# Optimization experiments

Measured on AMD Instinct MI355X. Metric: run time of the kernel, lower is better.

Reference implementation:

```python
import jax, jax.numpy as jnp
import numpy as np

WINDOW_SIZE = 128
NEG = -1e9

def setup_inputs() -> dict:
    key = jax.random.key(0)
    kq, kk, kv = jax.random.split(key, 3)
    B, H, T, D = 2, 16, 2048, 64
    q = jax.random.normal(kq, (B, H, T, D), dtype=jnp.float32)
    k = jax.random.normal(kk, (B, H, T, D), dtype=jnp.float32)
    v = jax.random.normal(kv, (B, H, T, D), dtype=jnp.float32)
    return {"q": q, "k": k, "v": v}

def reference(q, k, v):
    # q,k,v: (B, H, T, D)
    D = q.shape[-1]
    Tq, Tk = q.shape[2], k.shape[2]
    scale = 1.0 / jnp.sqrt(jnp.asarray(D, dtype=q.dtype))
    scores = jnp.einsum('bhqd,bhkd->bhqk', q, k) * scale  # (B,H,Tq,Tk)
    dist = jnp.abs(jnp.arange(Tq)[:, None] - jnp.arange(Tk)[None, :])
    window_mask = dist <= WINDOW_SIZE  # (Tq,Tk)
    scores = jnp.where(window_mask[None, None], scores, jnp.asarray(NEG, dtype=scores.dtype))
    attn = jax.nn.softmax(scores, axis=-1)
    output = jnp.einsum('bhqk,bhkd->bhqd', attn, v)
    return (output, attn)
```

## Files before the change

kernel.cpp:

```cpp
#include <hip/hip_runtime.h>
#include <hip/hip_bf16.h>

typedef short bf16x8 __attribute__((ext_vector_type(8)));
typedef short bf16x4 __attribute__((ext_vector_type(4)));
typedef float f32x4 __attribute__((ext_vector_type(4)));

#define T_DIM 2048
#define D_DIM 64
#define WIN 128
#define QBLK 64
#define ACCT 17
#define NEGBIG -1e30f

__device__ __forceinline__ short f2b(float x) {
  __hip_bfloat16 h = __float2bfloat16(x);
  return *reinterpret_cast<short*>(&h);
}
__device__ __forceinline__ float b2f(short s) {
  unsigned u = ((unsigned)(unsigned short)s) << 16;
  return __builtin_bit_cast(float, u);
}
__device__ __forceinline__ bf16x8 cvt8(f32x4 a, f32x4 b) {
  bf16x8 r;
  r[0] = f2b(a[0]); r[1] = f2b(a[1]); r[2] = f2b(a[2]); r[3] = f2b(a[3]);
  r[4] = f2b(b[0]); r[5] = f2b(b[1]); r[6] = f2b(b[2]); r[7] = f2b(b[3]);
  return r;
}
__device__ __forceinline__ int swz(int row, int b) { return row * 640 + (b ^ ((row & 7) << 4)); }

__global__ __launch_bounds__(256, 2) void lsa_one(
    const float* __restrict__ Qg, const float* __restrict__ Kg,
    const float* __restrict__ Vg, float* __restrict__ Og,
    float* __restrict__ Ag) {
  const int tid = threadIdx.x;
  const int work = ((blockIdx.x & 7) << 7) + (blockIdx.x >> 3);
  const int bh = work >> 5;
  const int q0 = (work & 31) * QBLK;
  int kstart = q0 - WIN; if (kstart < 0) kstart = 0;
  int kend = q0 + QBLK + WIN; if (kend > T_DIM) kend = T_DIM;
  const int KW = kend - kstart;
  const int nkt = KW >> 4;

  const float* qptr = Qg + (size_t)bh * (T_DIM * D_DIM);
  const float* kptr = Kg + (size_t)bh * (T_DIM * D_DIM);
  const float* vptr = Vg + (size_t)bh * (T_DIM * D_DIM);
  float* optr = Og + (size_t)bh * (T_DIM * D_DIM);
  float* aptr = Ag + (size_t)bh * ((size_t)T_DIM * T_DIM);

  __shared__ __align__(16) char Vb[D_DIM * 640];
  __shared__ __align__(16) char Pb[QBLK * 640];

  for (int idx = tid; idx < KW * 16; idx += 256) {
    const int r = idx >> 4, c4 = idx & 15;
    f32x4 f = *(const f32x4*)(vptr + (size_t)(kstart + r) * D_DIM + c4 * 4);
    const int d0 = c4 * 4;
    *(short*)(Vb + swz(d0 + 0, r * 2)) = f2b(f[0]);
    *(short*)(Vb + swz(d0 + 1, r * 2)) = f2b(f[1]);
    *(short*)(Vb + swz(d0 + 2, r * 2)) = f2b(f[2]);
    *(short*)(Vb + swz(d0 + 3, r * 2)) = f2b(f[3]);
  }

  const int lane = tid & 63, w = tid >> 6, c = lane & 15, hi = lane >> 4;

  const float* qrow = qptr + (size_t)(q0 + w * 16 + c) * D_DIM + 8 * hi;
  const bf16x8 qb0 = cvt8(*(const f32x4*)qrow, *(const f32x4*)(qrow + 4));
  const bf16x8 qb1 = cvt8(*(const f32x4*)(qrow + 32), *(const f32x4*)(qrow + 36));

  int klo = q0 + w * 16 - WIN - kstart; if (klo < 0) klo = 0;
  const int kt0 = klo >> 4;
  int kt1 = (q0 + w * 16 + 15 + WIN + 1 - kstart + 15) >> 4; if (kt1 > nkt) kt1 = nkt;
  const int s0 = kt0 >> 1, s1 = (kt1 + 1) >> 1;
  const int nlive = kt1 - kt0;

  f32x4 acc[ACCT];
#pragma unroll
  for (int i = 0; i < ACCT; ++i) {
    acc[i] = (f32x4){0.f, 0.f, 0.f, 0.f};
    if (i < nlive) {
      const float* kr = kptr + (size_t)(kstart + (kt0 + i) * 16 + c) * D_DIM + 8 * hi;
      const bf16x8 b0 = cvt8(*(const f32x4*)kr, *(const f32x4*)(kr + 4));
      const bf16x8 b1 = cvt8(*(const f32x4*)(kr + 32), *(const f32x4*)(kr + 36));
      acc[i] = __builtin_amdgcn_mfma_f32_16x16x32_bf16(b0, qb0, acc[i], 0, 0, 0);
      acc[i] = __builtin_amdgcn_mfma_f32_16x16x32_bf16(b1, qb1, acc[i], 0, 0, 0);
    }
  }

  {
    const f32x4 zv = {0.f, 0.f, 0.f, 0.f};
    for (int rr = 0; rr < 16; ++rr) {
      float* dst = aptr + (size_t)(q0 + w * 16 + rr) * T_DIM;
      for (int col = lane * 4; col < kstart; col += 256)
        __builtin_nontemporal_store(zv, (f32x4*)(dst + col));
      for (int col = kend + lane * 4; col < T_DIM; col += 256)
        __builtin_nontemporal_store(zv, (f32x4*)(dst + col));
    }
  }

  const int qr = q0 + w * 16 + c;
  const int kb = kstart + 4 * hi;
  float m = NEGBIG;
#pragma unroll
  for (int i = 0; i < ACCT; ++i)
    if (i < nlive) {
#pragma unroll
      for (int j = 0; j < 4; ++j) {
        float s = acc[i][j] * 0.125f;
        const int kcol = kb + (kt0 + i) * 16 + j;
        int dist = qr - kcol; dist = dist < 0 ? -dist : dist;
        s = (dist <= WIN) ? s : NEGBIG;
        acc[i][j] = s;
        m = fmaxf(m, s);
      }
    }
  m = fmaxf(m, __shfl_xor(m, 16));
  m = fmaxf(m, __shfl_xor(m, 32));
  float sum = 0.f;
#pragma unroll
  for (int i = 0; i < ACCT; ++i)
    if (i < nlive) {
#pragma unroll
      for (int j = 0; j < 4; ++j) {
        const float p = __expf(acc[i][j] - m);
        acc[i][j] = p;
        sum += p;
      }
    }
  sum += __shfl_xor(sum, 16);
  sum += __shfl_xor(sum, 32);
  const float inv = 1.f / sum;

  const int prow = w * 16 + c;
#pragma unroll
  for (int i = 0; i < ACCT; ++i)
    if (i < nlive) {
      bf16x4 pk;
#pragma unroll
      for (int j = 0; j < 4; ++j) pk[j] = f2b(acc[i][j] * inv);
      *(bf16x4*)(Pb + swz(prow, 32 * (kt0 + i) + 8 * hi)) = pk;
    }
  {
    const bf16x4 z4 = {0, 0, 0, 0};
    for (int t = 0; t < kt0; ++t) *(bf16x4*)(Pb + swz(prow, 32 * t + 8 * hi)) = z4;
    for (int t = kt1; t < nkt; ++t) *(bf16x4*)(Pb + swz(prow, 32 * t + 8 * hi)) = z4;
  }

  for (int rr = 0; rr < 16; ++rr) {
    const int r = w * 16 + rr;
    float* dst = aptr + (size_t)(q0 + r) * T_DIM + kstart;
#pragma unroll
    for (int i = 0; i < 5; ++i) {
      const int off = i * 256 + lane * 4;
      if (off < KW) {
        const bf16x4 pv = *(const bf16x4*)(Pb + swz(r, off * 2));
        f32x4 val;
        val[0] = b2f(pv[0]); val[1] = b2f(pv[1]); val[2] = b2f(pv[2]); val[3] = b2f(pv[3]);
        __builtin_nontemporal_store(val, (f32x4*)(dst + off));
      }
    }
  }

  __syncthreads();

  f32x4 ov[4];
#pragma unroll
  for (int dt = 0; dt < 4; ++dt) ov[dt] = (f32x4){0.f, 0.f, 0.f, 0.f};
  for (int s = s0; s < s1; ++s) {
    const bf16x8 pa = *(const bf16x8*)(Pb + swz(w * 16 + c, 64 * s + 16 * hi));
#pragma unroll
    for (int dt = 0; dt < 4; ++dt) {
      const bf16x8 vb = *(const bf16x8*)(Vb + swz(dt * 16 + c, 64 * s + 16 * hi));
      ov[dt] = __builtin_amdgcn_mfma_f32_16x16x32_bf16(pa, vb, ov[dt], 0, 0, 0);
    }
  }
#pragma unroll
  for (int dt = 0; dt < 4; ++dt)
#pragma unroll
    for (int j = 0; j < 4; ++j)
      __builtin_nontemporal_store(
          ov[dt][j], optr + (size_t)(q0 + w * 16 + 4 * hi + j) * D_DIM + dt * 16 + c);
}

extern "C" void kernel_launch(void* const* d_in, const int* in_sizes, int n_in,
                              void* d_out, int out_size, void* d_ws, size_t ws_size,
                              hipStream_t stream) {
  const float* q = (const float*)d_in[0];
  const float* k = (const float*)d_in[1];
  const float* v = (const float*)d_in[2];
  float* out = (float*)d_out;
  float* attn = out + (size_t)2 * 16 * T_DIM * D_DIM;
  lsa_one<<<dim3(2 * 16 * (T_DIM / QBLK)), dim3(256), 0, stream>>>(q, k, v, out, attn);
}
```

Measured before the change: 128.4 us.

## Keep probabilities in registers, store attn directly, feed PV MFMA from accumulators

Removes the shared-memory P buffer. The normalized attention rows are written straight from registers to global memory, and unnormalized bf16 probabilities feed a 16x16x16 MFMA directly from the score accumulator layout. Normalization by 1/sum is deferred to the output store using shuffles. Freeing the P buffer raises launch bounds to 4 blocks per SU, targeting occupancy and fewer LDS round trips. In exchange, the attn stores become 16-byte per-lane scattered writes rather than coalesced row writes, and the change adds manual s_nop hazard padding.

```diff
diff --git a/kernel.cpp b/kernel.cpp
--- a/kernel.cpp
+++ b/kernel.cpp
@@ -16,10 +16,6 @@
   __hip_bfloat16 h = __float2bfloat16(x);
   return *reinterpret_cast<short*>(&h);
 }
-__device__ __forceinline__ float b2f(short s) {
-  unsigned u = ((unsigned)(unsigned short)s) << 16;
-  return __builtin_bit_cast(float, u);
-}
 __device__ __forceinline__ bf16x8 cvt8(f32x4 a, f32x4 b) {
   bf16x8 r;
   r[0] = f2b(a[0]); r[1] = f2b(a[1]); r[2] = f2b(a[2]); r[3] = f2b(a[3]);
@@ -28,7 +24,19 @@
 }
 __device__ __forceinline__ int swz(int row, int b) { return row * 640 + (b ^ ((row & 7) << 4)); }
 
-__global__ __launch_bounds__(256, 2) void lsa_one(
+#if __has_builtin(__builtin_amdgcn_mfma_f32_16x16x16bf16_1k)
+__device__ __forceinline__ f32x4 mfma16(bf16x4 a, bf16x4 b, f32x4 c) {
+  return __builtin_amdgcn_mfma_f32_16x16x16bf16_1k(a, b, c, 0, 0, 0);
+}
+#else
+__device__ __forceinline__ f32x4 mfma16(bf16x4 a, bf16x4 b, f32x4 c) {
+  asm volatile("s_nop 1\n\tv_mfma_f32_16x16x16_bf16 %0, %1, %2, %0"
+               : "+v"(c) : "v"(a), "v"(b));
+  return c;
+}
+#endif
+
+__global__ __launch_bounds__(256, 4) void lsa_one(
     const float* __restrict__ Qg, const float* __restrict__ Kg,
     const float* __restrict__ Vg, float* __restrict__ Og,
     float* __restrict__ Ag) {
@@ -48,7 +56,6 @@
   float* aptr = Ag + (size_t)bh * ((size_t)T_DIM * T_DIM);
 
   __shared__ __align__(16) char Vb[D_DIM * 640];
-  __shared__ __align__(16) char Pb[QBLK * 640];
 
   for (int idx = tid; idx < KW * 16; idx += 256) {
     const int r = idx >> 4, c4 = idx & 15;
@@ -69,7 +76,6 @@
   int klo = q0 + w * 16 - WIN - kstart; if (klo < 0) klo = 0;
   const int kt0 = klo >> 4;
   int kt1 = (q0 + w * 16 + 15 + WIN + 1 - kstart + 15) >> 4; if (kt1 > nkt) kt1 = nkt;
-  const int s0 = kt0 >> 1, s1 = (kt1 + 1) >> 1;
   const int nlive = kt1 - kt0;
 
   f32x4 acc[ACCT];
@@ -129,34 +135,21 @@
   sum += __shfl_xor(sum, 32);
   const float inv = 1.f / sum;
 
-  const int prow = w * 16 + c;
+  {
+    float* brow = aptr + (size_t)(q0 + w * 16 + c) * T_DIM + kstart + 4 * hi;
 #pragma unroll
-  for (int i = 0; i < ACCT; ++i)
-    if (i < nlive) {
-      bf16x4 pk;
+    for (int i = 0; i < ACCT; ++i)
+      if (i < nlive) {
+        f32x4 v;
 #pragma unroll
-      for (int j = 0; j < 4; ++j) pk[j] = f2b(acc[i][j] * inv);
-      *(bf16x4*)(Pb + swz(prow, 32 * (kt0 + i) + 8 * hi)) = pk;
-    }
-  {
-    const bf16x4 z4 = {0, 0, 0, 0};
-    for (int t = 0; t < kt0; ++t) *(bf16x4*)(Pb + swz(prow, 32 * t + 8 * hi)) = z4;
-    for (int t = kt1; t < nkt; ++t) *(bf16x4*)(Pb + swz(prow, 32 * t + 8 * hi)) = z4;
-  }
-
-  for (int rr = 0; rr < 16; ++rr) {
-    const int r = w * 16 + rr;
-    float* dst = aptr + (size_t)(q0 + r) * T_DIM + kstart;
-#pragma unroll
-    for (int i = 0; i < 5; ++i) {
-      const int off = i * 256 + lane * 4;
-      if (off < KW) {
-        const bf16x4 pv = *(const bf16x4*)(Pb + swz(r, off * 2));
-        f32x4 val;
-        val[0] = b2f(pv[0]); val[1] = b2f(pv[1]); val[2] = b2f(pv[2]); val[3] = b2f(pv[3]);
-        __builtin_nontemporal_store(val, (f32x4*)(dst + off));
+        for (int j = 0; j < 4; ++j) v[j] = acc[i][j] * inv;
+        __builtin_nontemporal_store(v, (f32x4*)(brow + 16 * (kt0 + i)));
       }
-    }
+    const f32x4 zv = {0.f, 0.f, 0.f, 0.f};
+    for (int t = 0; t < kt0; ++t)
+      __builtin_nontemporal_store(zv, (f32x4*)(brow + 16 * t));
+    for (int t = kt1; t < nkt; ++t)
+      __builtin_nontemporal_store(zv, (f32x4*)(brow + 16 * t));
   }
 
   __syncthreads();
@@ -164,20 +157,31 @@
   f32x4 ov[4];
 #pragma unroll
   for (int dt = 0; dt < 4; ++dt) ov[dt] = (f32x4){0.f, 0.f, 0.f, 0.f};
-  for (int s = s0; s < s1; ++s) {
-    const bf16x8 pa = *(const bf16x8*)(Pb + swz(w * 16 + c, 64 * s + 16 * hi));
 #pragma unroll
-    for (int dt = 0; dt < 4; ++dt) {
-      const bf16x8 vb = *(const bf16x8*)(Vb + swz(dt * 16 + c, 64 * s + 16 * hi));
-      ov[dt] = __builtin_amdgcn_mfma_f32_16x16x32_bf16(pa, vb, ov[dt], 0, 0, 0);
+  for (int i = 0; i < ACCT; ++i)
+    if (i < nlive) {
+      bf16x4 pa;
+#pragma unroll
+      for (int j = 0; j < 4; ++j) pa[j] = f2b(acc[i][j]);
+      const int kb2 = (16 * (kt0 + i) + 4 * hi) * 2;
+#pragma unroll
+      for (int dt = 0; dt < 4; ++dt) {
+        const bf16x4 vb = *(const bf16x4*)(Vb + swz(dt * 16 + c, kb2));
+        ov[dt] = mfma16(pa, vb, ov[dt]);
+      }
     }
-  }
+  asm volatile("s_nop 7\n\ts_nop 7" :::);
+
+  float invq[4];
+#pragma unroll
+  for (int j = 0; j < 4; ++j) invq[j] = __shfl(inv, 4 * hi + j);
 #pragma unroll
   for (int dt = 0; dt < 4; ++dt)
 #pragma unroll
     for (int j = 0; j < 4; ++j)
       __builtin_nontemporal_store(
-          ov[dt][j], optr + (size_t)(q0 + w * 16 + 4 * hi + j) * D_DIM + dt * 16 + c);
+          ov[dt][j] * invq[j],
+          optr + (size_t)(q0 + w * 16 + 4 * hi + j) * D_DIM + dt * 16 + c);
 }
 
 extern "C" void kernel_launch(void* const* d_in, const int* in_sizes, int n_in,
```

New measurement: 148.2 us. +15.4%, slower.
